# Optimization experiments

Measured on AMD Instinct MI355X. Metric: run time of the kernel, lower is better.

Reference implementation:

```python
import jax, jax.numpy as jnp
import numpy as np

B, T, D, H = 4, 2048, 1024, 16
HD = D // H


def setup_inputs() -> dict:
    key = jax.random.key(0)
    ks = jax.random.split(key, 10)
    s = 1.0 / np.sqrt(D)
    # xavier_uniform bound for wbias [T,T]: sqrt(6/(T+T))
    wb_bound = float(np.sqrt(6.0 / (T + T)))
    return {
        "x": jax.random.normal(ks[0], (B, T, D), dtype=jnp.float32),
        "Wq": jax.random.normal(ks[1], (D, D), dtype=jnp.float32) * s,
        "bq": jnp.zeros((D,), dtype=jnp.float32),
        "Wk": jax.random.normal(ks[2], (D, D), dtype=jnp.float32) * s,
        "bk": jnp.zeros((D,), dtype=jnp.float32),
        "Wv": jax.random.normal(ks[3], (D, D), dtype=jnp.float32) * s,
        "bv": jnp.zeros((D,), dtype=jnp.float32),
        "Wo": jax.random.normal(ks[4], (D, D), dtype=jnp.float32) * s,
        "bo": jnp.zeros((D,), dtype=jnp.float32),
        "wbias": jax.random.uniform(ks[5], (T, T), dtype=jnp.float32,
                                    minval=-wb_bound, maxval=wb_bound),
    }


def reference(x, Wq, bq, Wk, bk, Wv, bv, Wo, bo, wbias):
    Bc, Tc, Dc = x.shape
    # projections, split heads: [B, H, T, HD]
    def proj(W, b):
        y = x @ W + b
        return y.reshape(Bc, Tc, H, HD).transpose(0, 2, 1, 3)

    Q = proj(Wq, bq)
    K = proj(Wk, bk)
    V = proj(Wv, bv)

    Q_sig = jax.nn.sigmoid(Q)
    eK = jnp.exp(K)                      # [B,H,T,HD]
    ew = jnp.exp(wbias[:Tc, :Tc])        # [T,T]

    num = jnp.einsum('ts,bhsd->bhtd', ew, eK * V)
    den = jnp.einsum('ts,bhsd->bhtd', ew, eK)
    out = Q_sig * (num / den)            # [B,H,T,HD]

    out = out.transpose(0, 2, 1, 3).reshape(Bc, Tc, Dc)
    return out @ Wo + bo
```

## Files before the change

### kernel.cpp

```cpp
#include <hip/hip_runtime.h>
#include <hip/hip_bf16.h>


#define AS1(p) ((const __attribute__((address_space(1))) void*)(p))
#define AS3(p) ((__attribute__((address_space(3))) void*)(p))

typedef _Float16 half8 __attribute__((ext_vector_type(8)));
typedef _Float16 half4v __attribute__((ext_vector_type(4)));
typedef float floatx16 __attribute__((ext_vector_type(16)));
typedef int intx4 __attribute__((ext_vector_type(4)));
typedef int intx8 __attribute__((ext_vector_type(8)));

__device__ __forceinline__ long frag_off(int r, int k) {
  return (long)(((((r >> 5) * 4 + (k >> 4)) * 2 + ((k >> 3) & 1)) * 32 + (r & 31)) * 8 + (k & 7));
}
__device__ __forceinline__ long off8(int r, int k) {
  return (long)((((((r >> 5) * 2 + ((k >> 6) & 1)) * 2 + ((k >> 4) & 1)) * 2 + ((k >> 5) & 1)) * 32 +
                 (r & 31)) * 16 + (k & 15));
}

__global__ __launch_bounds__(256) void prep_all(
    const float* __restrict__ x, const float* __restrict__ wb, const float* __restrict__ Wq,
    const float* __restrict__ Wk, const float* __restrict__ Wv, const float* __restrict__ Wo,
    _Float16* __restrict__ x_h, char* __restrict__ E8, _Float16* __restrict__ WqkvT,
    _Float16* __restrict__ WoT) {
  __shared__ _Float16 lds[64 * 132];
  const int bid = blockIdx.x;
  const int tid = threadIdx.x;

  if (bid < 1024) {
    const int tm = bid >> 4, tk = bid & 15;
    const long tbase = (long)bid * 8192;
#pragma unroll
    for (int p = 0; p < 4; ++p) {
      const int s = p * 256 + tid;
      const int r = ((s >> 8) << 5) + (s & 31);
      const int k = ((s >> 6) & 3) * 16 + ((s >> 5) & 1) * 8;
      const float* sp = x + (long)(tm * 128 + r) * 1024 + tk * 64 + k;
      const float4 v0 = *(const float4*)sp;
      const float4 v1 = *(const float4*)(sp + 4);
      half8 h;
      h[0] = (_Float16)v0.x; h[1] = (_Float16)v0.y; h[2] = (_Float16)v0.z; h[3] = (_Float16)v0.w;
      h[4] = (_Float16)v1.x; h[5] = (_Float16)v1.y; h[6] = (_Float16)v1.z; h[7] = (_Float16)v1.w;
      *(half8*)(x_h + tbase + (long)s * 8) = h;
    }
    return;
  }

  if (bid >= 1536) {
    const int e = bid - 1536;
    const int tt = e >> 4, ts = e & 15;
    char* dst = E8 + (long)e * 16384;
#pragma unroll
    for (int p = 0; p < 16; ++p) {
      const int idx = p * 256 + tid;
      const int r = idx >> 5, k = (idx & 31) * 4;
      const float4 v = *(const float4*)(wb + (long)(tt * 128 + r) * 2048 + ts * 128 + k);
      const float e0 = (__expf(v.x) - 1.0f) * 32.0f, e1 = (__expf(v.y) - 1.0f) * 32.0f;
      const float e2 = (__expf(v.z) - 1.0f) * 32.0f, e3 = (__expf(v.w) - 1.0f) * 32.0f;
      int pk = __builtin_amdgcn_cvt_pk_fp8_f32(e0, e1, 0, false);
      pk = __builtin_amdgcn_cvt_pk_fp8_f32(e2, e3, pk, true);
      *(int*)(dst + off8(r, k)) = pk;
    }
    return;
  }

  const int b2 = bid - 1024;
  const float* src0;
  const float* src1 = nullptr;
  _Float16* dst;
  int tn, tk, cb = 0;
  if (b2 < 128) {
    tn = b2 >> 4; tk = b2 & 15; src0 = Wq; dst = WqkvT;
  } else if (b2 < 384) {
    const int t = b2 - 128;
    tn = 8 + (t >> 4); tk = t & 15; cb = (tn - 8) * 64; src0 = Wk; src1 = Wv; dst = WqkvT;
  } else {
    const int t = b2 - 384;
    tn = t >> 4; tk = t & 15; src0 = Wo; dst = WoT;
  }
  if (!src1) {
#pragma unroll
    for (int p = 0; p < 8; ++p) {
      const int kl = p * 8 + (tid >> 5);
      const int cl = (tid & 31) * 4;
      const float4 v = *(const float4*)(src0 + (long)(tk * 64 + kl) * 1024 + tn * 128 + cl);
      half4v h;
      h[0] = (_Float16)v.x; h[1] = (_Float16)v.y; h[2] = (_Float16)v.z; h[3] = (_Float16)v.w;
      *(half4v*)(lds + kl * 132 + cl) = h;
    }
  } else {
#pragma unroll
    for (int m = 0; m < 2; ++m) {
      const float* s = m ? src1 : src0;
      const int rb = m ? 32 : 0;
#pragma unroll
      for (int p = 0; p < 4; ++p) {
        const int kl = p * 16 + (tid >> 4);
        const int cl = (tid & 15) * 4;
        const int rl = (cl >> 5) * 64 + rb + (cl & 31);
        const float4 v = *(const float4*)(s + (long)(tk * 64 + kl) * 1024 + cb + cl);
        half4v h;
        h[0] = (_Float16)v.x; h[1] = (_Float16)v.y; h[2] = (_Float16)v.z; h[3] = (_Float16)v.w;
        *(half4v*)(lds + kl * 132 + rl) = h;
      }
    }
  }
  __syncthreads();
  const long tbase = (long)(tn * 16 + tk) * 8192;
#pragma unroll
  for (int p = 0; p < 4; ++p) {
    const int s = p * 256 + tid;
    const int r = ((s >> 8) << 5) + (s & 31);
    const int kl = ((s >> 6) & 3) * 16 + ((s >> 5) & 1) * 8;
    half8 h;
#pragma unroll
    for (int j = 0; j < 8; ++j) h[j] = lds[(kl + j) * 132 + r];
    *(half8*)(dst + tbase + (long)s * 8) = h;
  }
}

template <int MODE>
__global__ __launch_bounds__(256) void gemm_bt(
    const _Float16* __restrict__ A, const _Float16* __restrict__ Bt, void* __restrict__ Cv,
    int Ktiles, const float* __restrict__ bias0, const float* __restrict__ bias1,
    const float* __restrict__ bias2, char* __restrict__ Zt8, float* __restrict__ cs) {
  __shared__ __align__(16) _Float16 sA[8192];
  __shared__ __align__(16) _Float16 sB[8192];
  const int tid = threadIdx.x;
  const int wave = tid >> 6, lane = tid & 63;
  const int l32 = lane & 31, khalf = lane >> 5;

  const int f = blockIdx.x + 64 * blockIdx.y;
  const int bxs = (f & 7) * 8 + ((f >> 3) & 7);
  const int bys = f >> 6;

  const int m0 = bxs * 128, n0 = bys * 128;
  const int wm = (wave >> 1) * 64, wn = (wave & 1) * 64;

  const _Float16* Atile = A + (long)bxs * Ktiles * 8192;
  const _Float16* Btile = Bt + (long)bys * Ktiles * 8192;

  floatx16 acc[2][2] = {};

  for (int tk = 0; tk < Ktiles; ++tk) {
    const _Float16* As = Atile + tk * 8192 + wave * 512 + lane * 8;
    const _Float16* Bs = Btile + tk * 8192 + wave * 512 + lane * 8;
#pragma unroll
    for (int c = 0; c < 4; ++c) {
      __builtin_amdgcn_global_load_lds(AS1(As + c * 2048), AS3(sA + c * 2048 + wave * 512), 16, 0, 0);
      __builtin_amdgcn_global_load_lds(AS1(Bs + c * 2048), AS3(sB + c * 2048 + wave * 512), 16, 0, 0);
    }
    __syncthreads();
#pragma unroll
    for (int ks = 0; ks < 4; ++ks) {
      half8 af[2], bf[2];
#pragma unroll
      for (int i = 0; i < 2; ++i) {
        af[i] = *(const half8*)(sA + (((wm >> 5) + i) * 4 + ks) * 512 + lane * 8);
        bf[i] = *(const half8*)(sB + (((wn >> 5) + i) * 4 + ks) * 512 + lane * 8);
      }
#pragma unroll
      for (int mt = 0; mt < 2; ++mt)
#pragma unroll
        for (int nt = 0; nt < 2; ++nt)
          acc[mt][nt] =
              __builtin_amdgcn_mfma_f32_32x32x16_f16(af[mt], bf[nt], acc[mt][nt], 0, 0, 0);
    }
    __syncthreads();
  }

  if (MODE == 0) {
    if (n0 < 1024) {
      _Float16* Qs = (_Float16*)Cv;
#pragma unroll
      for (int mt = 0; mt < 2; ++mt) {
        const long ttile = (m0 + wm + mt * 32) >> 5;
#pragma unroll
        for (int nt = 0; nt < 2; ++nt) {
          const int col = n0 + wn + nt * 32 + l32;
          const float bb = bias0[col];
          const long base = (ttile * 32 + (((n0 + wn) >> 5) + nt)) * 1024;
#pragma unroll
          for (int q = 0; q < 4; ++q) {
            half4v o;
#pragma unroll
            for (int rr = 0; rr < 4; ++rr) {
              const float v = acc[mt][nt][q * 4 + rr] + bb;
              o[rr] = (_Float16)(1.0f / (1.0f + __expf(-v)));
            }
            *(half4v*)(Qs + base + q * 256 + lane * 4) = o;
          }
        }
      }
    } else {
      const int g = (n0 - 1024 + wn) >> 6;
      const int ch = g * 32 + l32;
      const float bkc = bias1[ch], bvc = bias2[ch];
      const int jn = g * 64 + l32;
      const int b = m0 >> 11;
      char* Z8 = Zt8 + (long)b * 4194304 +
                 ((long)(jn >> 7) * 16 + ((m0 & 2047) >> 7)) * 16384;
      const int jnl = jn & 127;
      float sk = 0.f, sz = 0.f;
#pragma unroll
      for (int mt = 0; mt < 2; ++mt) {
#pragma unroll
        for (int q = 0; q < 4; ++q) {
          float ekv[4], ekk[4];
#pragma unroll
          for (int rr = 0; rr < 4; ++rr) {
            const float ek = __expf(acc[mt][0][q * 4 + rr] + bkc);
            const float vv = acc[mt][1][q * 4 + rr] + bvc;
            ekk[rr] = ek;
            ekv[rr] = ek * vv;
            sk += ek;
            sz += ek * vv;
          }
          const int sl = wm + mt * 32 + 4 * khalf + 8 * q;
          int pn = __builtin_amdgcn_cvt_pk_fp8_f32(ekv[0] * 0.25f, ekv[1] * 0.25f, 0, false);
          pn = __builtin_amdgcn_cvt_pk_fp8_f32(ekv[2] * 0.25f, ekv[3] * 0.25f, pn, true);
          int pd = __builtin_amdgcn_cvt_pk_fp8_f32(ekk[0] * 0.25f, ekk[1] * 0.25f, 0, false);
          pd = __builtin_amdgcn_cvt_pk_fp8_f32(ekk[2] * 0.25f, ekk[3] * 0.25f, pd, true);
          *(int*)(Z8 + off8(jnl, sl)) = pn;
          *(int*)(Z8 + off8(jnl + 32, sl)) = pd;
        }
      }
      atomicAdd(&cs[(long)b * 2048 + ch * 2], sz);
      atomicAdd(&cs[(long)b * 2048 + ch * 2 + 1], sk);
    }
    return;
  }

#pragma unroll
  for (int mt = 0; mt < 2; ++mt)
#pragma unroll
    for (int nt = 0; nt < 2; ++nt) {
      const int col = n0 + wn + nt * 32 + l32;
      const float bb = bias0[col];
#pragma unroll
      for (int reg = 0; reg < 16; ++reg) {
        const int row = m0 + wm + mt * 32 + 4 * khalf + 8 * (reg >> 2) + (reg & 3);
        ((float*)Cv)[(long)row * 1024 + col] = acc[mt][nt][reg] + bb;
      }
    }
}

__global__ __launch_bounds__(256) void gemm2_fp8(
    const char* __restrict__ E8, const char* __restrict__ Zt8, _Float16* __restrict__ OH,
    const _Float16* __restrict__ Qsig, const float* __restrict__ cs) {
  __shared__ __align__(16) char sA[16384];
  __shared__ __align__(16) char sB[16384];
  const int tid = threadIdx.x;
  const int wave = tid >> 6, lane = tid & 63;
  const int l32 = lane & 31, khalf = lane >> 5;

  const int f = blockIdx.x + 16 * (blockIdx.y + 16 * blockIdx.z);
  const int nid = (f & 7) * 128 + (f >> 3);
  const int bxs = nid & 15, bys = (nid >> 4) & 15, bzs = nid >> 8;

  const int m0 = bxs * 128, n0 = bys * 128;
  const int wm = (wave >> 1) * 64, wn = (wave & 1) * 64;

  const char* At = E8 + (long)bxs * 16 * 16384;
  const char* Bt = Zt8 + (long)bzs * 4194304 + (long)bys * 16 * 16384;

  floatx16 acc[2][2] = {};

  for (int tk = 0; tk < 16; ++tk) {
    const char* As = At + tk * 16384 + wave * 1024 + lane * 16;
    const char* Bs = Bt + tk * 16384 + wave * 1024 + lane * 16;
#pragma unroll
    for (int c = 0; c < 4; ++c) {
      __builtin_amdgcn_global_load_lds(AS1(As + c * 4096), AS3(sA + c * 4096 + wave * 1024), 16, 0, 0);
      __builtin_amdgcn_global_load_lds(AS1(Bs + c * 4096), AS3(sB + c * 4096 + wave * 1024), 16, 0, 0);
    }
    __syncthreads();
#pragma unroll
    for (int ks = 0; ks < 2; ++ks) {
      intx8 a8[2], b8[2];
#pragma unroll
      for (int i = 0; i < 2; ++i) {
        const char* pa = sA + (((wm >> 5) + i) * 2 + ks) * 2048 + khalf * 512 + l32 * 16;
        const intx4 alo = *(const intx4*)pa;
        const intx4 ahi = *(const intx4*)(pa + 1024);
        a8[i] = __builtin_shufflevector(alo, ahi, 0, 1, 2, 3, 4, 5, 6, 7);
        const char* pb = sB + (((wn >> 5) + i) * 2 + ks) * 2048 + khalf * 512 + l32 * 16;
        const intx4 blo = *(const intx4*)pb;
        const intx4 bhi = *(const intx4*)(pb + 1024);
        b8[i] = __builtin_shufflevector(blo, bhi, 0, 1, 2, 3, 4, 5, 6, 7);
      }
#pragma unroll
      for (int mt = 0; mt < 2; ++mt)
#pragma unroll
        for (int nt = 0; nt < 2; ++nt)
          acc[mt][nt] = __builtin_amdgcn_mfma_scale_f32_32x32x64_f8f6f4(
              a8[mt], b8[nt], acc[mt][nt], 0, 0, 0, 127u, 0, 127u);
    }
    __syncthreads();
  }

  const int ch = ((n0 + wn) >> 6) * 32 + l32;
  const float2 c2 = *(const float2*)(cs + (long)bzs * 2048 + ch * 2);
#pragma unroll
  for (int mt = 0; mt < 2; ++mt) {
    const long ttile = (long)(bzs * 2048 + m0 + wm + mt * 32) >> 5;
    const long qbase = (ttile * 32 + ((n0 + wn) >> 6)) * 1024;
#pragma unroll
    for (int q = 0; q < 4; ++q) {
      const half4v qv = *(const half4v*)(Qsig + qbase + q * 256 + lane * 4);
#pragma unroll
      for (int rr = 0; rr < 4; ++rr) {
        const int reg = q * 4 + rr;
        const float num = c2.x + acc[mt][0][reg] * 0.125f;
        const float den = c2.y + acc[mt][1][reg] * 0.125f;
        const int r = m0 + wm + mt * 32 + 4 * khalf + 8 * q + rr;
        const int R = bzs * 2048 + r;
        const long off = ((long)(R >> 7) * 16 + (ch >> 6)) * 8192 + frag_off(R & 127, ch & 63);
        OH[off] = (_Float16)((float)qv[rr] * num / den);
      }
    }
  }
}

extern "C" void kernel_launch(void* const* d_in, const int* in_sizes, int n_in, void* d_out,
                              int out_size, void* d_ws, size_t ws_size, hipStream_t stream) {
  const float* x = (const float*)d_in[0];
  const float* Wq = (const float*)d_in[1];
  const float* bq = (const float*)d_in[2];
  const float* Wk = (const float*)d_in[3];
  const float* bk = (const float*)d_in[4];
  const float* Wv = (const float*)d_in[5];
  const float* bv = (const float*)d_in[6];
  const float* Wo = (const float*)d_in[7];
  const float* bo = (const float*)d_in[8];
  const float* wb = (const float*)d_in[9];

  char* ws = (char*)d_ws;
  _Float16* x_h = (_Float16*)(ws + 0);
  _Float16* WqkvT = (_Float16*)(ws + 16777216);
  _Float16* WoT = (_Float16*)(ws + 23068672);
  char* E8 = (char*)(ws + 25165824);
  _Float16* Qsig = (_Float16*)(ws + 29360128);
  char* Zt8 = (char*)(ws + 46137344);
  _Float16* OutHead = (_Float16*)(ws + 62914560);
  float* cs = (float*)(ws + 79691776);

  hipMemsetAsync(cs, 0, 4 * 2048 * sizeof(float), stream);

  prep_all<<<1792, 256, 0, stream>>>(x, wb, Wq, Wk, Wv, Wo, x_h, E8, WqkvT, WoT);

  gemm_bt<0><<<dim3(64, 24), 256, 0, stream>>>(x_h, WqkvT, Qsig, 16, bq, bk, bv, Zt8, cs);

  gemm2_fp8<<<dim3(16, 16, 4), 256, 0, stream>>>(E8, Zt8, OutHead, Qsig, cs);

  gemm_bt<2><<<dim3(64, 8), 256, 0, stream>>>(OutHead, WoT, d_out, 16, bo, nullptr, nullptr,
                                              nullptr, nullptr);
}
```

Before: 255.9 us.

## Pipeline projection GEMMs with 4-slot LDS ring and 128x256 tiles

Replaces the single-buffered 128x128 GEMM with a 512-thread, 128x256-tile kernel that streams half-K-tile stages through a four-slot LDS ring, prefetching three stages ahead with explicit vmcnt waits and raised MFMA priority. The intent is to hide global-to-LDS latency behind MFMA work, which the old load-sync-compute-sync loop exposed, and to improve B reuse per block. In exchange it uses more LDS per block (96 KB), hardcodes K=1024, and relies on the epilogue indexing still matching the wider N tile.

```diff
diff --git a/kernel.cpp b/kernel.cpp
--- a/kernel.cpp
+++ b/kernel.cpp
@@ -120,55 +120,99 @@
   }
 }
 
+template <int VM>
+__device__ __forceinline__ void aft_phase(int g, const _Float16* __restrict__ Ablk,
+                                          const _Float16* __restrict__ Bblk,
+                                          _Float16* ring, int tid, int wid, int lane,
+                                          int wm, int wn, floatx16 (&acc)[2][2]) {
+  const _Float16* slotA = ring + (g & 3) * 4096;
+  const _Float16* slotB = ring + 16384 + (g & 3) * 8192;
+  half8 af[2][2], bf[2][2];
+#pragma unroll
+  for (int mt = 0; mt < 2; ++mt)
+#pragma unroll
+    for (int ks = 0; ks < 2; ++ks)
+      af[mt][ks] = *(const half8*)(slotA + ((wm >> 5) + mt) * 1024 + ks * 512 + lane * 8);
+#pragma unroll
+  for (int nt = 0; nt < 2; ++nt)
+#pragma unroll
+    for (int ks = 0; ks < 2; ++ks)
+      bf[nt][ks] = *(const half8*)(slotB + ((wn >> 5) + nt) * 1024 + ks * 512 + lane * 8);
+  const int gs = g + 3;
+  if (gs < 32) {
+    const int t = gs >> 1;
+    const long goff = (long)(tid >> 7) * 2048 + (gs & 1) * 1024 + (tid & 127) * 8;
+    _Float16* dA = ring + (gs & 3) * 4096 + wid * 512;
+    _Float16* dB = ring + 16384 + (gs & 3) * 8192 + wid * 512;
+    __builtin_amdgcn_global_load_lds(AS1(Ablk + (long)t * 8192 + goff), AS3(dA), 16, 0, 0);
+    __builtin_amdgcn_global_load_lds(AS1(Bblk + (long)t * 8192 + goff), AS3(dB), 16, 0, 0);
+    __builtin_amdgcn_global_load_lds(AS1(Bblk + (long)(16 + t) * 8192 + goff), AS3(dB + 4096),
+                                     16, 0, 0);
+  }
+  asm volatile("s_waitcnt vmcnt(%0)" ::"i"(VM) : "memory");
+  __builtin_amdgcn_s_barrier();
+  asm volatile("s_waitcnt lgkmcnt(0)" ::: "memory");
+  __builtin_amdgcn_s_setprio(1);
+#pragma unroll
+  for (int ks = 0; ks < 2; ++ks)
+#pragma unroll
+    for (int mt = 0; mt < 2; ++mt)
+#pragma unroll
+      for (int nt = 0; nt < 2; ++nt)
+        acc[mt][nt] =
+            __builtin_amdgcn_mfma_f32_32x32x16_f16(af[mt][ks], bf[nt][ks], acc[mt][nt], 0, 0, 0);
+  __builtin_amdgcn_s_setprio(0);
+  __builtin_amdgcn_s_barrier();
+  asm volatile("" ::: "memory");
+}
+
 template <int MODE>
-__global__ __launch_bounds__(256) void gemm_bt(
+__global__ __launch_bounds__(512, 2) void gemm_bt2(
     const _Float16* __restrict__ A, const _Float16* __restrict__ Bt, void* __restrict__ Cv,
-    int Ktiles, const float* __restrict__ bias0, const float* __restrict__ bias1,
+    const float* __restrict__ bias0, const float* __restrict__ bias1,
     const float* __restrict__ bias2, char* __restrict__ Zt8, float* __restrict__ cs) {
-  __shared__ __align__(16) _Float16 sA[8192];
-  __shared__ __align__(16) _Float16 sB[8192];
+  __shared__ __align__(16) _Float16 ring[49152];
   const int tid = threadIdx.x;
-  const int wave = tid >> 6, lane = tid & 63;
+  const int wid = tid >> 6, lane = tid & 63;
   const int l32 = lane & 31, khalf = lane >> 5;
 
-  const int f = blockIdx.x + 64 * blockIdx.y;
-  const int bxs = (f & 7) * 8 + ((f >> 3) & 7);
-  const int bys = f >> 6;
-
-  const int m0 = bxs * 128, n0 = bys * 128;
-  const int wm = (wave >> 1) * 64, wn = (wave & 1) * 64;
-
-  const _Float16* Atile = A + (long)bxs * Ktiles * 8192;
-  const _Float16* Btile = Bt + (long)bys * Ktiles * 8192;
+  const int f = blockIdx.x;
+  const int j = f >> 3;
+  const int bxs = (f & 7) * 8 + (j & 7);
+  const int bys = j >> 3;
+  const int m0 = bxs * 128, n0 = bys * 256;
+  const int wm = (wid >> 2) * 64, wn = (wid & 3) * 64;
+
+  const _Float16* Ablk = A + (long)bxs * 131072;
+  const _Float16* Bblk = Bt + (long)(bys * 2) * 131072;
+
+#pragma unroll
+  for (int g0 = 0; g0 < 3; ++g0) {
+    const int t = g0 >> 1;
+    const long goff = (long)(tid >> 7) * 2048 + (g0 & 1) * 1024 + (tid & 127) * 8;
+    __builtin_amdgcn_global_load_lds(AS1(Ablk + (long)t * 8192 + goff),
+                                     AS3(ring + g0 * 4096 + wid * 512), 16, 0, 0);
+    __builtin_amdgcn_global_load_lds(AS1(Bblk + (long)t * 8192 + goff),
+                                     AS3(ring + 16384 + g0 * 8192 + wid * 512), 16, 0, 0);
+    __builtin_amdgcn_global_load_lds(AS1(Bblk + (long)(16 + t) * 8192 + goff),
+                                     AS3(ring + 16384 + g0 * 8192 + 4096 + wid * 512), 16, 0, 0);
+  }
+  asm volatile("s_waitcnt vmcnt(6)" ::: "memory");
+  __builtin_amdgcn_s_barrier();
+  asm volatile("" ::: "memory");
 
   floatx16 acc[2][2] = {};
-
-  for (int tk = 0; tk < Ktiles; ++tk) {
-    const _Float16* As = Atile + tk * 8192 + wave * 512 + lane * 8;
-    const _Float16* Bs = Btile + tk * 8192 + wave * 512 + lane * 8;
-#pragma unroll
-    for (int c = 0; c < 4; ++c) {
-      __builtin_amdgcn_global_load_lds(AS1(As + c * 2048), AS3(sA + c * 2048 + wave * 512), 16, 0, 0);
-      __builtin_amdgcn_global_load_lds(AS1(Bs + c * 2048), AS3(sB + c * 2048 + wave * 512), 16, 0, 0);
-    }
-    __syncthreads();
-#pragma unroll
-    for (int ks = 0; ks < 4; ++ks) {
-      half8 af[2], bf[2];
-#pragma unroll
-      for (int i = 0; i < 2; ++i) {
-        af[i] = *(const half8*)(sA + (((wm >> 5) + i) * 4 + ks) * 512 + lane * 8);
-        bf[i] = *(const half8*)(sB + (((wn >> 5) + i) * 4 + ks) * 512 + lane * 8);
-      }
-#pragma unroll
-      for (int mt = 0; mt < 2; ++mt)
-#pragma unroll
-        for (int nt = 0; nt < 2; ++nt)
-          acc[mt][nt] =
-              __builtin_amdgcn_mfma_f32_32x32x16_f16(af[mt], bf[nt], acc[mt][nt], 0, 0, 0);
-    }
-    __syncthreads();
-  }
+#pragma unroll 1
+  for (int gb = 0; gb < 28; gb += 4) {
+    aft_phase<6>(gb + 0, Ablk, Bblk, ring, tid, wid, lane, wm, wn, acc);
+    aft_phase<6>(gb + 1, Ablk, Bblk, ring, tid, wid, lane, wm, wn, acc);
+    aft_phase<6>(gb + 2, Ablk, Bblk, ring, tid, wid, lane, wm, wn, acc);
+    aft_phase<6>(gb + 3, Ablk, Bblk, ring, tid, wid, lane, wm, wn, acc);
+  }
+  aft_phase<6>(28, Ablk, Bblk, ring, tid, wid, lane, wm, wn, acc);
+  aft_phase<3>(29, Ablk, Bblk, ring, tid, wid, lane, wm, wn, acc);
+  aft_phase<0>(30, Ablk, Bblk, ring, tid, wid, lane, wm, wn, acc);
+  aft_phase<0>(31, Ablk, Bblk, ring, tid, wid, lane, wm, wn, acc);
 
   if (MODE == 0) {
     if (n0 < 1024) {
@@ -194,10 +238,10 @@
         }
       }
     } else {
-      const int g = (n0 - 1024 + wn) >> 6;
-      const int ch = g * 32 + l32;
+      const int grp = (n0 - 1024 + wn) >> 6;
+      const int ch = grp * 32 + l32;
       const float bkc = bias1[ch], bvc = bias2[ch];
-      const int jn = g * 64 + l32;
+      const int jn = grp * 64 + l32;
       const int b = m0 >> 11;
       char* Z8 = Zt8 + (long)b * 4194304 +
                  ((long)(jn >> 7) * 16 + ((m0 & 2047) >> 7)) * 16384;
@@ -350,10 +394,9 @@
 
   prep_all<<<1792, 256, 0, stream>>>(x, wb, Wq, Wk, Wv, Wo, x_h, E8, WqkvT, WoT);
 
-  gemm_bt<0><<<dim3(64, 24), 256, 0, stream>>>(x_h, WqkvT, Qsig, 16, bq, bk, bv, Zt8, cs);
+  gemm_bt2<0><<<768, 512, 0, stream>>>(x_h, WqkvT, Qsig, bq, bk, bv, Zt8, cs);
 
   gemm2_fp8<<<dim3(16, 16, 4), 256, 0, stream>>>(E8, Zt8, OutHead, Qsig, cs);
 
-  gemm_bt<2><<<dim3(64, 8), 256, 0, stream>>>(OutHead, WoT, d_out, 16, bo, nullptr, nullptr,
-                                              nullptr, nullptr);
-}
+  gemm_bt2<2><<<256, 512, 0, stream>>>(OutHead, WoT, d_out, bo, nullptr, nullptr, nullptr, nullptr);
+}
```

Result: faster. 250.7 us (-2.0%).
